# Kernel optimization log

Measured on AMD Instinct MI355X. Metric: run time of the kernel, lower is better.

The kernel has to match this reference:

```python
import jax, jax.numpy as jnp
import numpy as np

NUM_HEADS = 16
HIDDEN = 1024
HEAD_DIM = HIDDEN // NUM_HEADS
B, S, D = 2, 2048, 1024


def setup_inputs() -> dict:
    key = jax.random.key(0)
    ks = jax.random.split(key, 7)
    scale = 1.0 / np.sqrt(D)
    return {
        "query": jax.random.normal(ks[0], (B, S, D), dtype=jnp.float32),
        "key": jax.random.normal(ks[1], (B, S, D), dtype=jnp.float32),
        "value": jax.random.normal(ks[2], (B, S, D), dtype=jnp.float32),
        "Wk_w": jax.random.normal(ks[3], (HIDDEN, D), dtype=jnp.float32) * scale,
        "Wk_b": jax.random.normal(ks[4], (HIDDEN,), dtype=jnp.float32) * scale,
        "Wv_w": jax.random.normal(ks[5], (HIDDEN, D), dtype=jnp.float32) * scale,
        "Wv_b": jax.random.normal(ks[6], (HIDDEN,), dtype=jnp.float32) * scale,
    }


def reference(query, key, value, Wk_w, Wk_b, Wv_w, Wv_b):
    # NOTE: in the original torch module, self.W_v is assigned twice, so the
    # SAME Linear (Wv) projects both key and value; Wk projects query.
    b, s, _ = query.shape

    def split_heads(x):  # [b,s,hidden] -> [b,h,s,hd]
        return x.reshape(b, s, NUM_HEADS, HEAD_DIM).transpose(0, 2, 1, 3)

    q = split_heads(query @ Wk_w.T + Wk_b)
    k = split_heads(key @ Wv_w.T + Wv_b)
    v = split_heads(value @ Wv_w.T + Wv_b)

    scores = jnp.einsum("bhqd,bhkd->bhqk", q, k) / jnp.sqrt(
        jnp.asarray(HEAD_DIM, dtype=q.dtype))
    probs = jax.nn.softmax(scores, axis=-1)
    out = jnp.einsum("bhqk,bhkd->bhqd", probs, v)
    return out.transpose(0, 2, 1, 3).reshape(b, s, NUM_HEADS * HEAD_DIM)
```

## Files before the change

kernel.cpp:

```cpp
#include <hip/hip_runtime.h>
#include <stdint.h>

typedef unsigned short u16;
typedef uint32_t u32;
typedef __bf16 bf16x8 __attribute__((ext_vector_type(8)));
typedef float f32x4 __attribute__((ext_vector_type(4)));
typedef float f32x16 __attribute__((ext_vector_type(16)));
typedef u16 u16x4 __attribute__((ext_vector_type(4)));
typedef u16 u16x8 __attribute__((ext_vector_type(8)));

#define XQ_OFF 0ul
#define XK_OFF 4194304ul
#define XV_OFF 8388608ul
#define WK_OFF 12582912ul
#define WV_OFF 13631488ul
#define Q_OFF  14680064ul
#define K_OFF  18874368ul
#define V_OFF  23068672ul

#define SCQ 0.18033688011112042f

#if __has_builtin(__builtin_amdgcn_exp2f)
#define EXP2F(x) __builtin_amdgcn_exp2f(x)
#else
#define EXP2F(x) exp2f(x)
#endif

__device__ __forceinline__ u16 f2bf(float f) {
  u32 u = __float_as_uint(f);
  u32 r = (u + 0x7fffu + ((u >> 16) & 1u)) >> 16;
  return (u16)r;
}

__device__ __forceinline__ u32 pk2(float a, float b) {
  typedef __bf16 bf2_t __attribute__((ext_vector_type(2)));
  typedef float f2_t __attribute__((ext_vector_type(2)));
  f2_t v; v[0] = a; v[1] = b;
  bf2_t h = __builtin_convertvector(v, bf2_t);
  union { bf2_t h; u32 u; } cv; cv.h = h; return cv.u;
}

__device__ __forceinline__ void load_lds16(const void* g, void* l) {
  __builtin_amdgcn_global_load_lds(
      (const __attribute__((address_space(1))) u32*)g,
      (__attribute__((address_space(3))) u32*)l, 16, 0, 0);
}

__device__ __forceinline__ u32 swz(u32 L) {
  return L ^ (((L >> 7) & 1u) << 4) ^ (((L >> 10) & 3u) << 5);
}

__global__ __launch_bounds__(256) void cvt_tile_kernel(
    const float* __restrict__ xq, const float* __restrict__ xk,
    const float* __restrict__ xv, const float* __restrict__ wk,
    const float* __restrict__ wv, u16* __restrict__ ws) {
  __shared__ u16 tile[4096];
  const int bid = blockIdx.x;
  const float* src; size_t dstbase; int rt, ktp;
  if (bid < 3072) {
    int m = bid >> 10, loc = bid & 1023;
    src = (m == 0) ? xq : (m == 1) ? xk : xv;
    dstbase = (size_t)m * 4194304ul;
    rt = loc >> 4; ktp = loc & 15;
  } else {
    int r2 = bid - 3072;
    int m = r2 >> 8, loc = r2 & 255;
    src = m ? wv : wk;
    dstbase = WK_OFF + (size_t)m * 1048576ul;
    rt = loc >> 4; ktp = loc & 15;
  }
  const int t = threadIdx.x;
  const int row0 = t >> 4, c = t & 15;
  const int k = c * 4;
  const float* s = src + (size_t)(rt * 64 + row0) * 1024ul + ktp * 64 + k;
#pragma unroll
  for (int i = 0; i < 4; ++i) {
    float4 v = *(const float4*)(s + (size_t)i * 16384ul);
    int row = row0 + i * 16;
    u32* p = (u32*)(tile + ((k >> 5) * 2048 + ((k >> 3) & 3) * 512 + row * 8 + (k & 7)));
    p[0] = pk2(v.x, v.y);
    p[1] = pk2(v.z, v.w);
  }
  __syncthreads();
  u16* dst = ws + dstbase + (size_t)(rt * 32 + ktp * 2) * 2048ul;
#pragma unroll
  for (int so = 0; so < 4096; so += 2048)
    *(u16x8*)(dst + so + t * 8) = *(const u16x8*)(tile + so + t * 8);
}

__global__ __launch_bounds__(256, 2) void proj_kernel(u16* __restrict__ ws,
                                                      const float* __restrict__ bk,
                                                      const float* __restrict__ bv) {
  const int proj = blockIdx.z;
  const int mtile = blockIdx.x;
  const int ntile = blockIdx.y;
  const u16* A = ws + (size_t)proj * 4194304ul;
  const u16* Bw = ws + ((proj == 0) ? WK_OFF : WV_OFF);
  const float* bias = (proj == 0) ? bk : bv;
  u16* outQ = ws + Q_OFF;
  u16* outK = ws + K_OFF;
  u16* outV = ws + V_OFF;

  const int t = threadIdx.x;
  const int w = t >> 6, lane = t & 63;
  const int wm = w >> 1, wn = w & 1;
  const int g = lane >> 4, c = lane & 15;

  __shared__ __align__(16) u16 smem[32768];

  const u16* Ag = A + (size_t)(2 * mtile) * 65536ul;
  const u16* Bg = Bw + (size_t)(2 * ntile) * 65536ul;
  const u32 t8 = (u32)t * 8u;
  const u32 so = swz((u32)t * 16u) >> 1;

  u32 poff[4];
#pragma unroll
  for (int mt = 0; mt < 4; ++mt)
    poff[mt] = swz((u32)((g << 10) | ((mt * 16 + c) << 4))) >> 1;

#define PSTAGE(buf, kt)                                            \
  do {                                                             \
    u16* bb = smem + (buf) * 8192;                                 \
    const size_t ko = (size_t)(kt) * 2048ul + so;                  \
    load_lds16(Ag + ko, bb + t8);                                  \
    load_lds16(Ag + 65536ul + ko, bb + 2048 + t8);                 \
    load_lds16(Bg + ko, bb + 4096 + t8);                           \
    load_lds16(Bg + 65536ul + ko, bb + 6144 + t8);                 \
  } while (0)

#define PFRAGS_MFMA(buf)                                                        \
  do {                                                                          \
    const u16* Ap = smem + (buf) * 8192 + wm * 2048;                            \
    const u16* Bp = smem + (buf) * 8192 + 4096 + wn * 2048;                     \
    bf16x8 af[4], bfv[4];                                                       \
    _Pragma("unroll") for (int mt = 0; mt < 4; ++mt)                            \
        af[mt] = *(const bf16x8*)(Ap + poff[mt]);                               \
    _Pragma("unroll") for (int nt = 0; nt < 4; ++nt)                            \
        bfv[nt] = *(const bf16x8*)(Bp + poff[nt]);                              \
    _Pragma("unroll") for (int mt = 0; mt < 4; ++mt)                            \
        _Pragma("unroll") for (int nt = 0; nt < 4; ++nt)                        \
            acc[mt][nt] = __builtin_amdgcn_mfma_f32_16x16x32_bf16(              \
                af[mt], bfv[nt], acc[mt][nt], 0, 0, 0);                         \
  } while (0)

  f32x4 acc[4][4];
#pragma unroll
  for (int mt = 0; mt < 4; ++mt)
#pragma unroll
    for (int nt = 0; nt < 4; ++nt) acc[mt][nt] = (f32x4){0.f, 0.f, 0.f, 0.f};

  PSTAGE(0, 0);
  PSTAGE(1, 1);
  PSTAGE(2, 2);
  PSTAGE(3, 3);

#pragma unroll 1
  for (int p = 0; p < 15; ++p) {
    asm volatile("s_waitcnt vmcnt(8)\n\ts_barrier" ::: "memory");
    const int b0 = (2 * p) & 3;
    PFRAGS_MFMA(b0);
    PFRAGS_MFMA(b0 + 1);
    __builtin_amdgcn_s_barrier();
    if (p < 14) {
      PSTAGE(b0, 2 * p + 4);
      PSTAGE(b0 + 1, 2 * p + 5);
    }
  }
  asm volatile("s_waitcnt vmcnt(0)\n\ts_barrier" ::: "memory");
  PFRAGS_MFMA(2);
  PFRAGS_MFMA(3);
#undef PSTAGE
#undef PFRAGS_MFMA

  const int m0 = mtile * 128 + wm * 64;
  const int n0 = ntile * 128 + wn * 64;
  if (proj == 2) {
#pragma unroll
    for (int nt = 0; nt < 4; ++nt) {
      const int col = n0 + nt * 16 + c;
      const float bvv = bias[col];
      const int h = col >> 6, d = col & 63;
#pragma unroll
      for (int mt = 0; mt < 4; ++mt) {
        const int mbase = m0 + mt * 16 + g * 4;
        const int b = mbase >> 11;
        const int bh = b * 16 + h;
        const int s = mbase & 2047;
        u16x4 pk;
#pragma unroll
        for (int r = 0; r < 4; ++r) pk[r] = f2bf(acc[mt][nt][r] + bvv);
        size_t idx = (size_t)bh * 131072ul + (size_t)(s >> 6) * 4096ul +
                     (size_t)((s & 63) >> 3) * 512ul + (size_t)d * 8ul + (size_t)(s & 7);
        *(u16x4*)(outV + idx) = pk;
      }
    }
  } else {
    __syncthreads();
    u16* Ew = smem + w * 4096;
#pragma unroll
    for (int nt = 0; nt < 4; ++nt) {
      const int d = nt * 16 + c;
      const float bvv = bias[n0 + nt * 16 + c];
#pragma unroll
      for (int mt = 0; mt < 4; ++mt) {
#pragma unroll
        for (int r = 0; r < 4; ++r) {
          const int srow = mt * 16 + g * 4 + r;
          float y = acc[mt][nt][r] + bvv;
          if (proj == 0) y *= SCQ;
          Ew[(d >> 3) * 512 + srow * 8 + (d & 7)] = f2bf(y);
        }
      }
    }
    __syncthreads();
    const int b = mtile >> 4;
    const int bh = b * 16 + ntile * 2 + wn;
    if (proj == 0) {
      u16* base = outQ + (size_t)bh * 131072ul + (size_t)(mtile & 15) * 8192ul + wm * 512;
#pragma unroll
      for (int i = 0; i < 8; ++i)
        *(u16x8*)(base + i * 1024 + lane * 8) = *(const u16x8*)(Ew + i * 512 + lane * 8);
    } else {
      u16* base = outK + (size_t)bh * 131072ul + (size_t)((mtile & 15) * 2 + wm) * 4096ul;
#pragma unroll
      for (int i = 0; i < 8; ++i)
        *(u16x8*)(base + i * 512 + lane * 8) = *(const u16x8*)(Ew + i * 512 + lane * 8);
    }
  }
}

__global__ __launch_bounds__(256, 2) void attn_kernel(const u16* __restrict__ ws,
                                                      float* __restrict__ out) {
  const int bh = blockIdx.x, qtile = blockIdx.y;
  const int b = bh >> 4, h = bh & 15;
  const int t = threadIdx.x, w = t >> 6, lane = t & 63;
  const int c32 = lane & 31, g2 = lane >> 5;

  __shared__ __align__(16) u16 Ks[4][4096];
  __shared__ __align__(16) u16 Vs[4][4096];

  const u16* Qg = ws + Q_OFF + (size_t)bh * 131072ul + (size_t)qtile * 8192ul;
  const u16* Kg = ws + K_OFF + (size_t)bh * 131072ul;
  const u16* Vg = ws + V_OFF + (size_t)bh * 131072ul;

  bf16x8 qf[4];
#pragma unroll
  for (int ks = 0; ks < 4; ++ks)
    qf[ks] = *(const bf16x8*)(Qg + (size_t)(ks * 2 + g2) * 1024ul +
                              (size_t)(w * 32 + c32) * 8ul);

  f32x16 O0, O1, Lacc, SA0, SA1, SB0, SB1;
#pragma unroll
  for (int i = 0; i < 16; ++i) { O0[i] = 0.f; O1[i] = 0.f; Lacc[i] = 0.f; }

#define STAGE_KV(buf, jj)                                        \
  do {                                                           \
    const u16* Kj = Kg + (size_t)(jj) * 4096ul;                  \
    const u16* Vj = Vg + (size_t)(jj) * 4096ul;                  \
    load_lds16(Kj + (size_t)t * 8ul, &Ks[buf][t * 8]);           \
    load_lds16(Kj + 2048ul + (size_t)t * 8ul, &Ks[buf][2048 + t * 8]); \
    load_lds16(Vj + (size_t)t * 8ul, &Vs[buf][t * 8]);           \
    load_lds16(Vj + 2048ul + (size_t)t * 8ul, &Vs[buf][2048 + t * 8]); \
  } while (0)

#define QK_CHUNK(Kb, S0v, S1v)                                               \
  do {                                                                       \
    _Pragma("unroll") for (int i = 0; i < 16; ++i) { S0v[i] = 0.f; S1v[i] = 0.f; } \
    __builtin_amdgcn_s_setprio(1);                                           \
    _Pragma("unroll") for (int ks = 0; ks < 4; ++ks) {                       \
      bf16x8 kf0 = *(const bf16x8*)((Kb) + (ks * 2 + g2) * 512 + c32 * 8);   \
      bf16x8 kf1 = *(const bf16x8*)((Kb) + (ks * 2 + g2) * 512 + (32 + c32) * 8); \
      S0v = __builtin_amdgcn_mfma_f32_32x32x16_bf16(kf0, qf[ks], S0v, 0, 0, 0); \
      S1v = __builtin_amdgcn_mfma_f32_32x32x16_bf16(kf1, qf[ks], S1v, 0, 0, 0); \
    }                                                                        \
    __builtin_amdgcn_s_setprio(0);                                           \
  } while (0)

#define SOFTPV(S0v, S1v, Vb)                                                 \
  do {                                                                       \
    _Pragma("unroll") for (int i = 0; i < 16; ++i) {                         \
      S0v[i] = EXP2F(S0v[i]); S1v[i] = EXP2F(S1v[i]);                        \
    }                                                                        \
    Lacc += S0v;                                                             \
    Lacc += S1v;                                                             \
    u32 pa[4][4];                                                            \
    _Pragma("unroll") for (int half = 0; half < 2; ++half) {                 \
      const f32x16& Sx = half ? S1v : S0v;                                   \
      _Pragma("unroll") for (int sub = 0; sub < 2; ++sub) {                  \
        const int rb = sub * 8;                                              \
        u32 q0 = pk2(Sx[rb + 0], Sx[rb + 1]);                                \
        u32 q1 = pk2(Sx[rb + 2], Sx[rb + 3]);                                \
        u32 q2 = pk2(Sx[rb + 4], Sx[rb + 5]);                                \
        u32 q3 = pk2(Sx[rb + 6], Sx[rb + 7]);                                \
        asm volatile("v_permlane32_swap_b32 %0, %1" : "+v"(q0), "+v"(q2));   \
        asm volatile("v_permlane32_swap_b32 %0, %1" : "+v"(q1), "+v"(q3));   \
        const int kstep = half * 2 + sub;                                    \
        pa[kstep][0] = q0; pa[kstep][1] = q1;                                \
        pa[kstep][2] = q2; pa[kstep][3] = q3;                                \
      }                                                                      \
    }                                                                        \
    __builtin_amdgcn_s_setprio(1);                                           \
    _Pragma("unroll") for (int kstep = 0; kstep < 4; ++kstep) {              \
      union { u32 u[4]; bf16x8 b; } pcv;                                     \
      _Pragma("unroll") for (int i = 0; i < 4; ++i) pcv.u[i] = pa[kstep][i]; \
      bf16x8 vf0 = *(const bf16x8*)((Vb) + (kstep * 2 + g2) * 512 + c32 * 8); \
      bf16x8 vf1 = *(const bf16x8*)((Vb) + (kstep * 2 + g2) * 512 + (32 + c32) * 8); \
      O0 = __builtin_amdgcn_mfma_f32_32x32x16_bf16(pcv.b, vf0, O0, 0, 0, 0); \
      O1 = __builtin_amdgcn_mfma_f32_32x32x16_bf16(pcv.b, vf1, O1, 0, 0, 0); \
    }                                                                        \
    __builtin_amdgcn_s_setprio(0);                                           \
  } while (0)

  STAGE_KV(0, 0);
  STAGE_KV(1, 1);
  STAGE_KV(2, 2);
  asm volatile("s_waitcnt vmcnt(8)\n\ts_barrier" ::: "memory");
  QK_CHUNK(Ks[0], SA0, SA1);

#pragma unroll 1
  for (int jj = 0; jj < 15; ++jj) {
    const int j = 2 * jj;
    asm volatile("s_waitcnt vmcnt(4)\n\ts_barrier" ::: "memory");
    if (j + 3 < 32) STAGE_KV((j + 3) & 3, j + 3);
    QK_CHUNK(Ks[(j + 1) & 3], SB0, SB1);
    SOFTPV(SA0, SA1, Vs[j & 3]);
    asm volatile("s_waitcnt vmcnt(4)\n\ts_barrier" ::: "memory");
    if (j + 4 < 32) STAGE_KV((j + 4) & 3, j + 4);
    QK_CHUNK(Ks[(j + 2) & 3], SA0, SA1);
    SOFTPV(SB0, SB1, Vs[(j + 1) & 3]);
  }
  asm volatile("s_waitcnt vmcnt(0)\n\ts_barrier" ::: "memory");
  QK_CHUNK(Ks[3], SB0, SB1);
  SOFTPV(SA0, SA1, Vs[2]);
  SOFTPV(SB0, SB1, Vs[3]);
#undef STAGE_KV
#undef QK_CHUNK
#undef SOFTPV

  float lp = 0.f;
#pragma unroll
  for (int i = 0; i < 16; ++i) lp += Lacc[i];
  float lA = lp, lB = lp;
  asm volatile("v_permlane32_swap_b32 %0, %1" : "+v"(lA), "+v"(lB));
  const float Ltot = lA + lB;

  const int q0 = qtile * 128 + w * 32;
  float* outb = out + (size_t)(b * 2048 + q0) * 1024ul + h * 64 + c32;
#pragma unroll
  for (int r = 0; r < 16; ++r) {
    const int qr = (r & 3) + 8 * (r >> 2) + 4 * g2;
    int lv = __builtin_amdgcn_ds_bpermute(qr << 2, __float_as_int(Ltot));
    const float inv = 1.0f / __int_as_float(lv);
    float* rp = outb + (size_t)qr * 1024ul;
    rp[0] = O0[r] * inv;
    rp[32] = O1[r] * inv;
  }
}

extern "C" void kernel_launch(void* const* d_in, const int* in_sizes, int n_in,
                              void* d_out, int out_size, void* d_ws, size_t ws_size,
                              hipStream_t stream) {
  const float* q = (const float*)d_in[0];
  const float* k = (const float*)d_in[1];
  const float* v = (const float*)d_in[2];
  const float* wk = (const float*)d_in[3];
  const float* bk = (const float*)d_in[4];
  const float* wv = (const float*)d_in[5];
  const float* bv = (const float*)d_in[6];
  u16* ws = (u16*)d_ws;
  float* out = (float*)d_out;

  cvt_tile_kernel<<<3584, 256, 0, stream>>>(q, k, v, wk, wv, ws);
  proj_kernel<<<dim3(32, 8, 3), 256, 0, stream>>>(ws, bk, bv);
  attn_kernel<<<dim3(32, 16), 256, 0, stream>>>(ws, out);
}
```

Before: 172.9 us.

## Process two query tiles per wave to reuse K/V fragments, halve attention grid

Each wave now handles 64 queries (two 32-row tiles) instead of 32, so each block covers 256 queries and the grid halves to 256 blocks. K and V fragments are loaded from LDS once into registers and reused for both query tiles, which halves LDS reads and global K/V staging per query. The software pipeline that overlapped the QK of the next chunk with softmax/PV of the current one is replaced by a simpler per-chunk body. The occupancy hint drops to one block per SIMD set because register use rises. With 256 blocks on a 256-CU device, each CU gets a single block, which reduces latency hiding.

Measured after the change: 194.2 us. 12.3% more time.

```diff
diff --git a/kernel.cpp b/kernel.cpp
--- a/kernel.cpp
+++ b/kernel.cpp
@@ -229,9 +229,9 @@
   }
 }
 
-__global__ __launch_bounds__(256, 2) void attn_kernel(const u16* __restrict__ ws,
+__global__ __launch_bounds__(256, 1) void attn_kernel(const u16* __restrict__ ws,
                                                       float* __restrict__ out) {
-  const int bh = blockIdx.x, qtile = blockIdx.y;
+  const int bh = blockIdx.x, qb = blockIdx.y;
   const int b = bh >> 4, h = bh & 15;
   const int t = threadIdx.x, w = t >> 6, lane = t & 63;
   const int c32 = lane & 31, g2 = lane >> 5;
@@ -239,19 +239,29 @@
   __shared__ __align__(16) u16 Ks[4][4096];
   __shared__ __align__(16) u16 Vs[4][4096];
 
-  const u16* Qg = ws + Q_OFF + (size_t)bh * 131072ul + (size_t)qtile * 8192ul;
+  const u16* Qg = ws + Q_OFF + (size_t)bh * 131072ul;
   const u16* Kg = ws + K_OFF + (size_t)bh * 131072ul;
   const u16* Vg = ws + V_OFF + (size_t)bh * 131072ul;
 
-  bf16x8 qf[4];
-#pragma unroll
-  for (int ks = 0; ks < 4; ++ks)
-    qf[ks] = *(const bf16x8*)(Qg + (size_t)(ks * 2 + g2) * 1024ul +
-                              (size_t)(w * 32 + c32) * 8ul);
-
-  f32x16 O0, O1, Lacc, SA0, SA1, SB0, SB1;
-#pragma unroll
-  for (int i = 0; i < 16; ++i) { O0[i] = 0.f; O1[i] = 0.f; Lacc[i] = 0.f; }
+  bf16x8 qf0[4], qf1[4];
+  {
+    const int qa0 = qb * 256 + w * 64 + c32;
+    const int qa1 = qa0 + 32;
+    const size_t o0 = (size_t)(qa0 >> 7) * 8192ul + (size_t)(qa0 & 127) * 8ul;
+    const size_t o1 = (size_t)(qa1 >> 7) * 8192ul + (size_t)(qa1 & 127) * 8ul;
+#pragma unroll
+    for (int ks = 0; ks < 4; ++ks) {
+      qf0[ks] = *(const bf16x8*)(Qg + o0 + (size_t)(ks * 2 + g2) * 1024ul);
+      qf1[ks] = *(const bf16x8*)(Qg + o1 + (size_t)(ks * 2 + g2) * 1024ul);
+    }
+  }
+
+  f32x16 O0a, O1a, La, O0b, O1b, Lb;
+#pragma unroll
+  for (int i = 0; i < 16; ++i) {
+    O0a[i] = 0.f; O1a[i] = 0.f; La[i] = 0.f;
+    O0b[i] = 0.f; O1b[i] = 0.f; Lb[i] = 0.f;
+  }
 
 #define STAGE_KV(buf, jj)                                        \
   do {                                                           \
@@ -263,27 +273,13 @@
     load_lds16(Vj + 2048ul + (size_t)t * 8ul, &Vs[buf][2048 + t * 8]); \
   } while (0)
 
-#define QK_CHUNK(Kb, S0v, S1v)                                               \
-  do {                                                                       \
-    _Pragma("unroll") for (int i = 0; i < 16; ++i) { S0v[i] = 0.f; S1v[i] = 0.f; } \
-    __builtin_amdgcn_s_setprio(1);                                           \
-    _Pragma("unroll") for (int ks = 0; ks < 4; ++ks) {                       \
-      bf16x8 kf0 = *(const bf16x8*)((Kb) + (ks * 2 + g2) * 512 + c32 * 8);   \
-      bf16x8 kf1 = *(const bf16x8*)((Kb) + (ks * 2 + g2) * 512 + (32 + c32) * 8); \
-      S0v = __builtin_amdgcn_mfma_f32_32x32x16_bf16(kf0, qf[ks], S0v, 0, 0, 0); \
-      S1v = __builtin_amdgcn_mfma_f32_32x32x16_bf16(kf1, qf[ks], S1v, 0, 0, 0); \
-    }                                                                        \
-    __builtin_amdgcn_s_setprio(0);                                           \
-  } while (0)
-
-#define SOFTPV(S0v, S1v, Vb)                                                 \
+#define SM_PACK(S0v, S1v, LaccV, paV)                                        \
   do {                                                                       \
     _Pragma("unroll") for (int i = 0; i < 16; ++i) {                         \
       S0v[i] = EXP2F(S0v[i]); S1v[i] = EXP2F(S1v[i]);                        \
     }                                                                        \
-    Lacc += S0v;                                                             \
-    Lacc += S1v;                                                             \
-    u32 pa[4][4];                                                            \
+    LaccV += S0v;                                                            \
+    LaccV += S1v;                                                            \
     _Pragma("unroll") for (int half = 0; half < 2; ++half) {                 \
       const f32x16& Sx = half ? S1v : S0v;                                   \
       _Pragma("unroll") for (int sub = 0; sub < 2; ++sub) {                  \
@@ -295,65 +291,102 @@
         asm volatile("v_permlane32_swap_b32 %0, %1" : "+v"(q0), "+v"(q2));   \
         asm volatile("v_permlane32_swap_b32 %0, %1" : "+v"(q1), "+v"(q3));   \
         const int kstep = half * 2 + sub;                                    \
-        pa[kstep][0] = q0; pa[kstep][1] = q1;                                \
-        pa[kstep][2] = q2; pa[kstep][3] = q3;                                \
+        paV[kstep][0] = q0; paV[kstep][1] = q1;                              \
+        paV[kstep][2] = q2; paV[kstep][3] = q3;                              \
       }                                                                      \
     }                                                                        \
+  } while (0)
+
+#define PV_TILE(paV, O0v, O1v)                                               \
+  do {                                                                       \
     __builtin_amdgcn_s_setprio(1);                                           \
     _Pragma("unroll") for (int kstep = 0; kstep < 4; ++kstep) {              \
       union { u32 u[4]; bf16x8 b; } pcv;                                     \
-      _Pragma("unroll") for (int i = 0; i < 4; ++i) pcv.u[i] = pa[kstep][i]; \
-      bf16x8 vf0 = *(const bf16x8*)((Vb) + (kstep * 2 + g2) * 512 + c32 * 8); \
-      bf16x8 vf1 = *(const bf16x8*)((Vb) + (kstep * 2 + g2) * 512 + (32 + c32) * 8); \
-      O0 = __builtin_amdgcn_mfma_f32_32x32x16_bf16(pcv.b, vf0, O0, 0, 0, 0); \
-      O1 = __builtin_amdgcn_mfma_f32_32x32x16_bf16(pcv.b, vf1, O1, 0, 0, 0); \
+      _Pragma("unroll") for (int i = 0; i < 4; ++i) pcv.u[i] = paV[kstep][i]; \
+      O0v = __builtin_amdgcn_mfma_f32_32x32x16_bf16(pcv.b, vfr0[kstep], O0v, 0, 0, 0); \
+      O1v = __builtin_amdgcn_mfma_f32_32x32x16_bf16(pcv.b, vfr1[kstep], O1v, 0, 0, 0); \
     }                                                                        \
     __builtin_amdgcn_s_setprio(0);                                           \
+  } while (0)
+
+#define BODY(buf)                                                            \
+  do {                                                                       \
+    const u16* Kb = Ks[buf];                                                 \
+    const u16* Vb = Vs[buf];                                                 \
+    bf16x8 kfr0[4], kfr1[4];                                                 \
+    _Pragma("unroll") for (int ks = 0; ks < 4; ++ks) {                       \
+      kfr0[ks] = *(const bf16x8*)(Kb + (ks * 2 + g2) * 512 + c32 * 8);       \
+      kfr1[ks] = *(const bf16x8*)(Kb + (ks * 2 + g2) * 512 + (32 + c32) * 8); \
+    }                                                                        \
+    f32x16 SA0, SA1, SB0, SB1;                                               \
+    _Pragma("unroll") for (int i = 0; i < 16; ++i) {                         \
+      SA0[i] = 0.f; SA1[i] = 0.f; SB0[i] = 0.f; SB1[i] = 0.f;                \
+    }                                                                        \
+    __builtin_amdgcn_s_setprio(1);                                           \
+    _Pragma("unroll") for (int ks = 0; ks < 4; ++ks) {                       \
+      SA0 = __builtin_amdgcn_mfma_f32_32x32x16_bf16(kfr0[ks], qf0[ks], SA0, 0, 0, 0); \
+      SA1 = __builtin_amdgcn_mfma_f32_32x32x16_bf16(kfr1[ks], qf0[ks], SA1, 0, 0, 0); \
+    }                                                                        \
+    _Pragma("unroll") for (int ks = 0; ks < 4; ++ks) {                       \
+      SB0 = __builtin_amdgcn_mfma_f32_32x32x16_bf16(kfr0[ks], qf1[ks], SB0, 0, 0, 0); \
+      SB1 = __builtin_amdgcn_mfma_f32_32x32x16_bf16(kfr1[ks], qf1[ks], SB1, 0, 0, 0); \
+    }                                                                        \
+    __builtin_amdgcn_s_setprio(0);                                           \
+    bf16x8 vfr0[4], vfr1[4];                                                 \
+    _Pragma("unroll") for (int kstep = 0; kstep < 4; ++kstep) {              \
+      vfr0[kstep] = *(const bf16x8*)(Vb + (kstep * 2 + g2) * 512 + c32 * 8); \
+      vfr1[kstep] = *(const bf16x8*)(Vb + (kstep * 2 + g2) * 512 + (32 + c32) * 8); \
+    }                                                                        \
+    u32 paA[4][4], paB[4][4];                                                \
+    SM_PACK(SA0, SA1, La, paA);               \
+    PV_TILE(paA, O0a, O1a);                                                  \
+    SM_PACK(SB0, SB1, Lb, paB);               \
+    PV_TILE(paB, O0b, O1b);                                                  \
   } while (0)
 
   STAGE_KV(0, 0);
   STAGE_KV(1, 1);
   STAGE_KV(2, 2);
-  asm volatile("s_waitcnt vmcnt(8)\n\ts_barrier" ::: "memory");
-  QK_CHUNK(Ks[0], SA0, SA1);
 
 #pragma unroll 1
-  for (int jj = 0; jj < 15; ++jj) {
-    const int j = 2 * jj;
-    asm volatile("s_waitcnt vmcnt(4)\n\ts_barrier" ::: "memory");
-    if (j + 3 < 32) STAGE_KV((j + 3) & 3, j + 3);
-    QK_CHUNK(Ks[(j + 1) & 3], SB0, SB1);
-    SOFTPV(SA0, SA1, Vs[j & 3]);
-    asm volatile("s_waitcnt vmcnt(4)\n\ts_barrier" ::: "memory");
-    if (j + 4 < 32) STAGE_KV((j + 4) & 3, j + 4);
-    QK_CHUNK(Ks[(j + 2) & 3], SA0, SA1);
-    SOFTPV(SB0, SB1, Vs[(j + 1) & 3]);
-  }
+  for (int j = 0; j < 30; ++j) {
+    asm volatile("s_waitcnt vmcnt(8)\n\ts_barrier" ::: "memory");
+    if (j < 29) STAGE_KV((j + 3) & 3, j + 3);
+    BODY(j & 3);
+  }
+  asm volatile("s_waitcnt vmcnt(4)\n\ts_barrier" ::: "memory");
+  BODY(2);
   asm volatile("s_waitcnt vmcnt(0)\n\ts_barrier" ::: "memory");
-  QK_CHUNK(Ks[3], SB0, SB1);
-  SOFTPV(SA0, SA1, Vs[2]);
-  SOFTPV(SB0, SB1, Vs[3]);
+  BODY(3);
 #undef STAGE_KV
-#undef QK_CHUNK
-#undef SOFTPV
-
-  float lp = 0.f;
-#pragma unroll
-  for (int i = 0; i < 16; ++i) lp += Lacc[i];
-  float lA = lp, lB = lp;
-  asm volatile("v_permlane32_swap_b32 %0, %1" : "+v"(lA), "+v"(lB));
-  const float Ltot = lA + lB;
-
-  const int q0 = qtile * 128 + w * 32;
-  float* outb = out + (size_t)(b * 2048 + q0) * 1024ul + h * 64 + c32;
-#pragma unroll
-  for (int r = 0; r < 16; ++r) {
-    const int qr = (r & 3) + 8 * (r >> 2) + 4 * g2;
-    int lv = __builtin_amdgcn_ds_bpermute(qr << 2, __float_as_int(Ltot));
-    const float inv = 1.0f / __int_as_float(lv);
-    float* rp = outb + (size_t)qr * 1024ul;
-    rp[0] = O0[r] * inv;
-    rp[32] = O1[r] * inv;
+#undef SM_PACK
+#undef PV_TILE
+#undef BODY
+
+  const int q0base = qb * 256 + w * 64;
+#pragma unroll
+  for (int tile = 0; tile < 2; ++tile) {
+    const f32x16& Lc = tile ? Lb : La;
+    const f32x16& O0 = tile ? O0b : O0a;
+    const f32x16& O1 = tile ? O1b : O1a;
+    float lp = 0.f;
+#pragma unroll
+    for (int i = 0; i < 16; ++i) lp += Lc[i];
+    float lA = lp, lB = lp;
+    asm volatile("v_permlane32_swap_b32 %0, %1" : "+v"(lA), "+v"(lB));
+    const float Ltot = lA + lB;
+
+    const int q0 = q0base + tile * 32;
+    float* outb = out + (size_t)(b * 2048 + q0) * 1024ul + h * 64 + c32;
+#pragma unroll
+    for (int r = 0; r < 16; ++r) {
+      const int qr = (r & 3) + 8 * (r >> 2) + 4 * g2;
+      int lv = __builtin_amdgcn_ds_bpermute(qr << 2, __float_as_int(Ltot));
+      const float inv = 1.0f / __int_as_float(lv);
+      float* rp = outb + (size_t)qr * 1024ul;
+      rp[0] = O0[r] * inv;
+      rp[32] = O1[r] * inv;
+    }
   }
 }
 
@@ -372,5 +405,5 @@
 
   cvt_tile_kernel<<<3584, 256, 0, stream>>>(q, k, v, wk, wv, ws);
   proj_kernel<<<dim3(32, 8, 3), 256, 0, stream>>>(ws, bk, bv);
-  attn_kernel<<<dim3(32, 16), 256, 0, stream>>>(ws, out);
-}
+  attn_kernel<<<dim3(32, 8), 256, 0, stream>>>(ws, out);
+}
```
